# Optimization experiments

Hardware: AMD Instinct MI355X
Metric: run time of the kernel (lower is better)

## Reference

```python
import jax, jax.numpy as jnp
import numpy as np

S, HID = 2048, 4096
H, KV, D = 32, 8, 128
EPS = 1e-6
THETA = 10000.0


def setup_inputs() -> dict:
    key = jax.random.key(0)
    k0, k1, k2 = jax.random.split(key, 3)
    return {
        "positions": jnp.arange(S, dtype=jnp.int32),
        "hidden_states": jax.random.normal(k0, (S, HID), jnp.float32),
        "w_qkv": jax.random.normal(k1, ((H + 2 * KV) * D, HID), jnp.float32) * 0.02,
        "w_o": jax.random.normal(k2, (HID, H * D), jnp.float32) * 0.02,
        "gq": jnp.ones((D,), jnp.float32),
        "gk": jnp.ones((D,), jnp.float32),
    }


def _rmsnorm(x, g):
    # per-head RMSNorm over last dim (head_dim)
    return x * jax.lax.rsqrt(jnp.mean(x * x, axis=-1, keepdims=True) + EPS) * g


def _rope(x, positions):
    # NeoX-style rotary embedding, rotary_dim == head_dim
    half = D // 2
    inv_freq = 1.0 / (THETA ** (jnp.arange(half, dtype=jnp.float32) * 2.0 / D))
    freqs = positions.astype(jnp.float32)[:, None] * inv_freq  # [S, half]
    cos = jnp.cos(freqs)[:, None, :]  # [S, 1, half]
    sin = jnp.sin(freqs)[:, None, :]
    x1, x2 = x[..., :half], x[..., half:]
    return jnp.concatenate([x1 * cos - x2 * sin, x2 * cos + x1 * sin], axis=-1)


def reference(positions, hidden_states, w_qkv, w_o, gq, gk):
    qkv = hidden_states @ w_qkv.T  # [S, (H+2KV)*D]
    q = qkv[:, : H * D].reshape(S, H, D)
    k = qkv[:, H * D : (H + KV) * D].reshape(S, KV, D)
    v = qkv[:, (H + KV) * D :].reshape(S, KV, D)

    q = _rmsnorm(q, gq)
    k = _rmsnorm(k, gk)
    q = _rope(q, positions)
    k = _rope(k, positions)

    rep = H // KV
    kf = jnp.repeat(k, rep, axis=1)  # [S, H, D]
    vf = jnp.repeat(v, rep, axis=1)

    scale = D ** -0.5
    scores = jnp.einsum("qhd,khd->hqk", q, kf) * scale  # [H, S, S]
    causal = jnp.tril(jnp.ones((S, S), dtype=bool))
    scores = jnp.where(causal[None], scores, jnp.finfo(scores.dtype).min)
    attn = jax.nn.softmax(scores, axis=-1)
    ctx = jnp.einsum("hqk,khd->qhd", attn, vf).reshape(S, H * D)
    return ctx @ w_o.T  # [S, HID]
```

## Files before the change

### kernel.cpp

```cpp
#include <hip/hip_runtime.h>
#include <hip/hip_bf16.h>

#define S_LEN 2048
#define HID   4096
#define NH    32
#define NKV   8
#define DH    128
#define NQKV  ((NH + 2*NKV) * DH)

typedef __attribute__((ext_vector_type(8))) short s16x8;
typedef __attribute__((ext_vector_type(4))) short s16x4;
typedef __attribute__((ext_vector_type(4))) float f32x4;

__device__ __forceinline__ short f2bf(float x) {
    union { __hip_bfloat16 b; short s; } u;
    u.b = __float2bfloat16(x);
    return u.s;
}
__device__ __forceinline__ float bf2f(short s) {
    union { unsigned int u; float f; } v;
    v.u = ((unsigned int)(unsigned short)s) << 16;
    return v.f;
}

__device__ __forceinline__ void gload16(const void* g, void* l) {
    __builtin_amdgcn_global_load_lds(
        (const __attribute__((address_space(1))) void*)g,
        (__attribute__((address_space(3))) void*)l,
        16, 0, 0);
}

__device__ __forceinline__ void cstore(float* p, float v) { *p = v; }
__device__ __forceinline__ void cstore(short* p, float v) { *p = f2bf(v); }

#define ROPE_C (13.287712379549449f / 64.0f)

__global__ __launch_bounds__(256) void convert_hs_wqkv(
        const float* __restrict__ hs, short* __restrict__ hsp,
        const float* __restrict__ wq, short* __restrict__ wqb,
        const int* __restrict__ pos, float* __restrict__ cst)
{
    const int bid = blockIdx.x;
    if (bid < 1536) {
        const long n = (long)NQKV * HID;
        long i0 = ((long)bid * 256 + threadIdx.x) * 4;
        long stride = 1536L * 256 * 4;
        for (long i = i0; i < n; i += stride) {
            float4 v = *(const float4*)(wq + i);
            s16x4 o;
            o[0] = f2bf(v.x); o[1] = f2bf(v.y); o[2] = f2bf(v.z); o[3] = f2bf(v.w);
            *(s16x4*)(wqb + i) = o;
        }
        return;
    }
    if (bid < 2048) {
        const int nchunk = (S_LEN / 16) * (HID / 32) * 64;
        for (int c = (bid - 1536) * 256 + threadIdx.x; c < nchunk; c += 512 * 256) {
            int lane = c & 63, k32 = (c >> 6) & 127, m16 = c >> 13;
            int row = m16 * 16 + (lane & 15);
            int k   = k32 * 32 + (lane >> 4) * 8;
            const float4* p = (const float4*)(hs + (long)row * HID + k);
            float4 v0 = p[0], v1 = p[1];
            s16x8 o;
            o[0] = f2bf(v0.x); o[1] = f2bf(v0.y); o[2] = f2bf(v0.z); o[3] = f2bf(v0.w);
            o[4] = f2bf(v1.x); o[5] = f2bf(v1.y); o[6] = f2bf(v1.z); o[7] = f2bf(v1.w);
            *(s16x8*)(hsp + (long)c * 8) = o;
        }
        return;
    }
    const int idx = (bid - 2048) * 256 + threadIdx.x;
    const int s = idx >> 3, j0 = (idx & 7) * 8;
    const float po = (float)pos[s];
#pragma unroll
    for (int jj = 0; jj < 8; ++jj) {
        int j = j0 + jj;
        float ang = po * exp2f(-(float)j * ROPE_C);
        float2 cs;
        cs.x = cosf(ang);
        cs.y = sinf(ang);
        *(float2*)(cst + ((long)s * 64 + j) * 2) = cs;
    }
}

template <typename OT>
__global__ __launch_bounds__(256, 2) void gemm192(
        const short* __restrict__ Ap, const short* __restrict__ B,
        OT* __restrict__ C, int M, int N, int K)
{
    __shared__ char lds[49152];
    const int t = threadIdx.x;
    const int w = t >> 6, l = t & 63, g = l >> 4, q16 = l & 15;
    const int wm = w >> 1, wn = w & 1;
    const int bx = blockIdx.x, by = blockIdx.y;
    const int NT = K >> 6;

    const int srow = t >> 3;
    const int schunk = (t & 7) ^ (srow & 7);
    unsigned goffB[6];
#pragma unroll
    for (int i = 0; i < 6; ++i)
        goffB[i] = (unsigned)(((bx * 192 + i * 32 + srow) * K) * 2 + schunk * 16);
    const int dstw = w * 1024;

    auto STAGE = [&](int kt) {
        char* dB = lds + (kt & 1) * 24576 + dstw;
        const unsigned kb = (unsigned)kt * 128;
#pragma unroll
        for (int i = 0; i < 6; ++i)
            gload16((const char*)B + (goffB[i] + kb), dB + i * 4096);
    };

    unsigned aBase[4];
#pragma unroll
    for (int mi = 0; mi < 4; ++mi)
        aBase[mi] = ((unsigned)((by * 8 + wm * 4 + mi) * 128) * 64 + (unsigned)l) * 16;

    int boff[6];
#pragma unroll
    for (int ni = 0; ni < 6; ++ni) boff[ni] = (wn * 96 + ni * 16 + q16) * 128;
    const int sw0 = ((g) ^ (q16 & 7)) << 4;
    const int sw1 = ((4 + g) ^ (q16 & 7)) << 4;

    f32x4 acc[4][6] = {};
    s16x8 aE[4][2], aO[4][2], b0E[2][2], b0O[2][2], b1[4][2];

    STAGE(0);
    __builtin_amdgcn_sched_barrier(0);
#pragma unroll
    for (int mi = 0; mi < 4; ++mi)
#pragma unroll
        for (int kk = 0; kk < 2; ++kk)
            aE[mi][kk] = *(const s16x8*)((const char*)Ap + aBase[mi] + kk * 1024);
    __builtin_amdgcn_sched_barrier(0);
    STAGE(1);
    asm volatile("s_waitcnt vmcnt(6)" ::: "memory");
    __builtin_amdgcn_s_barrier();
    {
        const char* B0 = lds;
#pragma unroll
        for (int ni = 0; ni < 2; ++ni) {
            b0E[ni][0] = *(const s16x8*)(B0 + boff[ni] + sw0);
            b0E[ni][1] = *(const s16x8*)(B0 + boff[ni] + sw1);
        }
        asm volatile("s_waitcnt lgkmcnt(0)" ::: "memory");
        __builtin_amdgcn_sched_barrier(0);
    }

#define GB(KT, AC, AN, B0C, B0N, PAR) do {                                    \
                    \
    const char* Bc_ = lds + (PAR) * 24576;                                    \
    _Pragma("unroll")                                                         \
    for (int ni = 0; ni < 4; ++ni) {                                          \
        b1[ni][0] = *(const s16x8*)(Bc_ + boff[2 + ni] + sw0);                \
        b1[ni][1] = *(const s16x8*)(Bc_ + boff[2 + ni] + sw1);                \
    }                                                                         \
    __builtin_amdgcn_sched_barrier(0);                                        \
    __builtin_amdgcn_s_setprio(1);                                            \
    _Pragma("unroll")                                                         \
    for (int mi = 0; mi < 4; ++mi)                                            \
    _Pragma("unroll")                                                         \
    for (int ni = 0; ni < 2; ++ni)                                            \
    _Pragma("unroll")                                                         \
    for (int kk = 0; kk < 2; ++kk)                                            \
        acc[mi][ni] = __builtin_amdgcn_mfma_f32_16x16x32_bf16(                \
                AC[mi][kk], B0C[ni][kk], acc[mi][ni], 0, 0, 0);               \
    __builtin_amdgcn_s_setprio(0);                                            \
               \
    asm volatile("s_waitcnt lgkmcnt(0)" ::: "memory");                        \
    __builtin_amdgcn_sched_barrier(0);                                        \
    asm volatile("s_waitcnt vmcnt(0)" ::: "memory");                          \
    __builtin_amdgcn_s_barrier();                                             \
         \
    if ((KT) + 1 < NT) {                                                      \
        _Pragma("unroll")                                                     \
        for (int mi = 0; mi < 4; ++mi)                                        \
        _Pragma("unroll")                                                     \
        for (int kk = 0; kk < 2; ++kk)                                        \
            AN[mi][kk] = *(const s16x8*)((const char*)Ap + aBase[mi]          \
                    + (((KT) + 1) * 2 + kk) * 1024);                          \
    }                                                                         \
    __builtin_amdgcn_sched_barrier(0);                                        \
    if ((KT) + 2 < NT) STAGE((KT) + 2);                                       \
    if ((KT) + 1 < NT) {                                                      \
        const char* Bn_ = lds + ((PAR) ^ 1) * 24576;                          \
        _Pragma("unroll")                                                     \
        for (int ni = 0; ni < 2; ++ni) {                                      \
            B0N[ni][0] = *(const s16x8*)(Bn_ + boff[ni] + sw0);               \
            B0N[ni][1] = *(const s16x8*)(Bn_ + boff[ni] + sw1);               \
        }                                                                     \
    }                                                                         \
    __builtin_amdgcn_sched_barrier(0);                                        \
                                             \
    __builtin_amdgcn_s_setprio(1);                                            \
    _Pragma("unroll")                                                         \
    for (int mi = 0; mi < 4; ++mi)                                            \
    _Pragma("unroll")                                                         \
    for (int ni = 0; ni < 4; ++ni)                                            \
    _Pragma("unroll")                                                         \
    for (int kk = 0; kk < 2; ++kk)                                            \
        acc[mi][2 + ni] = __builtin_amdgcn_mfma_f32_16x16x32_bf16(            \
                AC[mi][kk], b1[ni][kk], acc[mi][2 + ni], 0, 0, 0);            \
    __builtin_amdgcn_s_setprio(0);                                            \
         \
    asm volatile("s_waitcnt lgkmcnt(0)" ::: "memory");                        \
    __builtin_amdgcn_sched_barrier(0);                                        \
    if ((KT) + 2 < NT) asm volatile("s_waitcnt vmcnt(6)" ::: "memory");       \
    else               asm volatile("s_waitcnt vmcnt(0)" ::: "memory");       \
    __builtin_amdgcn_sched_barrier(0);                                        \
} while (0)

    for (int kt = 0; kt < NT; kt += 2) {
        GB(kt,     aE, aO, b0E, b0O, 0);
        GB(kt + 1, aO, aE, b0O, b0E, 1);
    }
#undef GB

#pragma unroll
    for (int mi = 0; mi < 4; ++mi) {
        long row = (long)by * 128 + wm * 64 + mi * 16 + g * 4;
#pragma unroll
        for (int ni = 0; ni < 6; ++ni) {
            long col = (long)bx * 192 + wn * 96 + ni * 16 + q16;
            f32x4 v = acc[mi][ni];
#pragma unroll
            for (int r = 0; r < 4; ++r)
                cstore(&C[(row + r) * (long)N + col], v[r]);
        }
    }
}

template <typename OT>
__global__ __launch_bounds__(256, 2) void gemm_bt(
        const short* __restrict__ A, const short* __restrict__ B,
        OT* __restrict__ C, int M, int N, int K)
{
    __shared__ char lds[65536];
    const int t = threadIdx.x;
    const int w = t >> 6, l = t & 63, g = l >> 4, q16 = l & 15;
    const int wm = w >> 1, wn = w & 1;
    const int bx = blockIdx.x, by = blockIdx.y;
    const int NT = K >> 6;

    const int srow = t >> 3;
    const int schunk = (t & 7) ^ (srow & 7);
    unsigned goffA[4], goffB[4];
#pragma unroll
    for (int i = 0; i < 4; ++i) {
        goffA[i] = (unsigned)(((by * 128 + i * 32 + srow) * K) * 2 + schunk * 16);
        goffB[i] = (unsigned)(((bx * 128 + i * 32 + srow) * K) * 2 + schunk * 16);
    }
    const int dstw = w * 1024;

    auto STAGE = [&](int kt) {
        const int par = kt & 1;
        char* dA = lds + par * 16384 + dstw;
        char* dB = lds + 32768 + par * 16384 + dstw;
        const unsigned kb = (unsigned)kt * 128;
#pragma unroll
        for (int i = 0; i < 4; ++i) {
            gload16((const char*)A + (goffA[i] + kb), dA + i * 4096);
            gload16((const char*)B + (goffB[i] + kb), dB + i * 4096);
        }
    };

    int aoff[4], boff[4];
#pragma unroll
    for (int i = 0; i < 4; ++i) {
        aoff[i] = (wm * 64 + i * 16 + q16) * 128;
        boff[i] = (wn * 64 + i * 16 + q16) * 128;
    }
    const int sw0 = ((g) ^ (q16 & 7)) << 4;
    const int sw1 = ((4 + g) ^ (q16 & 7)) << 4;

    f32x4 acc[4][4] = {};
    s16x8 aE[4][2], aO[4][2], bf[4][2];

    STAGE(0); STAGE(1);
    asm volatile("s_waitcnt vmcnt(8)" ::: "memory");
    __builtin_amdgcn_s_barrier();
    {
        const char* A0 = lds;
#pragma unroll
        for (int mi = 0; mi < 4; ++mi) {
            aE[mi][0] = *(const s16x8*)(A0 + aoff[mi] + sw0);
            aE[mi][1] = *(const s16x8*)(A0 + aoff[mi] + sw1);
        }
    }

#define GB(KT, AC, AN, PAR) do {                                              \
    const char* Bs_ = lds + 32768 + (PAR) * 16384;                            \
    _Pragma("unroll")                                                         \
    for (int ni = 0; ni < 4; ++ni) {                                          \
        bf[ni][0] = *(const s16x8*)(Bs_ + boff[ni] + sw0);                    \
        bf[ni][1] = *(const s16x8*)(Bs_ + boff[ni] + sw1);                    \
    }                                                                         \
    asm volatile("s_waitcnt lgkmcnt(4)" ::: "memory");      \
    __builtin_amdgcn_sched_barrier(0);                                        \
    __builtin_amdgcn_s_setprio(1);                                            \
    _Pragma("unroll")                                                         \
    for (int mi = 0; mi < 4; ++mi)                                            \
    _Pragma("unroll")                                                         \
    for (int ni = 0; ni < 2; ++ni)                                            \
    _Pragma("unroll")                                                         \
    for (int kk = 0; kk < 2; ++kk)                                            \
        acc[mi][ni] = __builtin_amdgcn_mfma_f32_16x16x32_bf16(                \
                AC[mi][kk], bf[ni][kk], acc[mi][ni], 0, 0, 0);                \
    __builtin_amdgcn_s_setprio(0);                                            \
    asm volatile("s_waitcnt lgkmcnt(0)" ::: "memory");          \
    __builtin_amdgcn_sched_barrier(0);                                        \
    asm volatile("s_waitcnt vmcnt(0)" ::: "memory");        \
    __builtin_amdgcn_s_barrier();       \
    if ((KT) + 2 < NT) STAGE((KT) + 2);                                       \
    if ((KT) + 1 < NT) {                      \
        const char* An_ = lds + (((PAR) ^ 1) * 16384);                        \
        _Pragma("unroll")                                                     \
        for (int mi = 0; mi < 4; ++mi) {                                      \
            AN[mi][0] = *(const s16x8*)(An_ + aoff[mi] + sw0);                \
            AN[mi][1] = *(const s16x8*)(An_ + aoff[mi] + sw1);                \
        }                                                                     \
    }                                                                         \
    __builtin_amdgcn_s_setprio(1);                                            \
    _Pragma("unroll")                                                         \
    for (int mi = 0; mi < 4; ++mi)                                            \
    _Pragma("unroll")                                                         \
    for (int ni = 0; ni < 2; ++ni)                                            \
    _Pragma("unroll")                                                         \
    for (int kk = 0; kk < 2; ++kk)                                            \
        acc[mi][2 + ni] = __builtin_amdgcn_mfma_f32_16x16x32_bf16(            \
                AC[mi][kk], bf[2 + ni][kk], acc[mi][2 + ni], 0, 0, 0);        \
    __builtin_amdgcn_s_setprio(0);                                            \
} while (0)

    for (int kt = 0; kt < NT; kt += 2) {
        GB(kt,     aE, aO, 0);
        GB(kt + 1, aO, aE, 1);
    }
#undef GB

#pragma unroll
    for (int mi = 0; mi < 4; ++mi) {
        long row = (long)by * 128 + wm * 64 + mi * 16 + g * 4;
#pragma unroll
        for (int ni = 0; ni < 4; ++ni) {
            long col = (long)bx * 128 + wn * 64 + ni * 16 + q16;
            f32x4 v = acc[mi][ni];
#pragma unroll
            for (int r = 0; r < 4; ++r)
                cstore(&C[(row + r) * (long)N + col], v[r]);
        }
    }
}

__global__ __launch_bounds__(256) void post_gemm1_fused(
        const short* __restrict__ qkvb, const float* __restrict__ cst,
        const float* __restrict__ gk,
        short* __restrict__ ko, short* __restrict__ vt)
{
    const int bid = blockIdx.x;

    if (bid < 2048) {
        const int s = bid;
        const int slot = NH + (threadIdx.x >> 5);
        const int p = threadIdx.x & 31, d = p * 4;

        s16x4 xv = *(const s16x4*)(qkvb + (long)s * NQKV + slot * DH + d);
        float x[4];
#pragma unroll
        for (int r = 0; r < 4; ++r) x[r] = bf2f(xv[r]);

        float ss = x[0]*x[0] + x[1]*x[1] + x[2]*x[2] + x[3]*x[3];
#pragma unroll
        for (int o = 1; o < 32; o <<= 1) ss += __shfl_xor(ss, o);
        float rms = rsqrtf(ss * (1.0f / DH) + 1e-6f);

        float y[4];
#pragma unroll
        for (int r = 0; r < 4; ++r) y[r] = x[r] * rms * gk[d + r];

        float y2[4];
#pragma unroll
        for (int r = 0; r < 4; ++r) y2[r] = __shfl_xor(y[r], 16);

        const int jbase = d & 63;
        s16x4 ov;
#pragma unroll
        for (int r = 0; r < 4; ++r) {
            float2 cs = *(const float2*)(cst + ((long)s * 64 + jbase + r) * 2);
            float outv = (d < 64) ? (y[r] * cs.x - y2[r] * cs.y)
                                  : (y[r] * cs.x + y2[r] * cs.y);
            ov[r] = f2bf(outv);
        }
        *(s16x4*)(ko + ((long)s * NKV + (slot - NH)) * DH + d) = ov;
        return;
    }

    __shared__ short tile[64][72];
    const int idx2 = bid - 2048;
    const int sb = idx2 & 31, db = (idx2 >> 5) & 1, h = idx2 >> 6;
    const int t = threadIdx.x;
#pragma unroll
    for (int i = 0; i < 2; ++i) {
        int c = i * 256 + t;
        int row = c >> 3, dc = (c & 7) * 8;
        const short* src = qkvb + (long)(sb*64 + row) * NQKV
                           + (NH + NKV + h) * DH + db*64 + dc;
        s16x8 x = *(const s16x8*)src;
#pragma unroll
        for (int jj = 0; jj < 8; ++jj) tile[row][dc + jj] = x[jj];
    }
    __syncthreads();
#pragma unroll
    for (int i = 0; i < 2; ++i) {
        int c = i * 256 + t;
        int dr = c >> 3, sc = (c & 7) * 8;
        s16x8 y;
#pragma unroll
        for (int jj = 0; jj < 8; ++jj) y[jj] = tile[sc + jj][dr];
        short* dst = vt + (long)(h*DH + db*64 + dr) * S_LEN + sb*64 + sc;
        *(s16x8*)dst = y;
    }
}

__device__ __forceinline__ void stage_kv(const char* kgB, const char* vgB,
                                         int kt, int t, char* kd, char* vd)
{
    const int w = t >> 6;
#pragma unroll
    for (int ci = 0; ci < 4; ++ci) {
        int c = ci * 256 + t;
        int row = c >> 4, col16 = c & 15;
        const char* gk = kgB + (long)(kt*64 + row) * (NKV*DH*2)
                         + ((col16*16) ^ ((row & 7) << 4));
        gload16(gk, kd + ci*4096 + w*1024);
        int rowv = c >> 3, scol8 = c & 7;
        const char* gv = vgB + (long)rowv * (S_LEN*2) + kt*128
                         + ((scol8*16) ^ ((rowv & 7) << 4));
        gload16(gv, vd + ci*4096 + w*1024);
    }
}

__global__ __launch_bounds__(256, 2) void attn_kernel(
        const float* __restrict__ wo, short* __restrict__ wob,
        const short* __restrict__ qkvb, const float* __restrict__ cst,
        const float* __restrict__ gq,
        const short* __restrict__ kg, const short* __restrict__ vtg,
        short* __restrict__ ctx)
{
    const int bx = blockIdx.x;
    if (bx >= 512) {
        const long n = (long)HID * (NH * DH);
        long i0 = ((long)(bx - 512) * 256 + threadIdx.x) * 4;
        long stride = 2048L * 256 * 4;
        for (long i = i0; i < n; i += stride) {
            float4 v = *(const float4*)(wo + i);
            s16x4 o;
            o[0] = f2bf(v.x); o[1] = f2bf(v.y); o[2] = f2bf(v.z); o[3] = f2bf(v.w);
            *(s16x4*)(wob + i) = o;
        }
        return;
    }

    const int h  = bx & 31;
    const int slot = bx >> 5;
    const int qb = (slot < 8) ? slot : 23 - slot;
    const int kvh = h >> 2;
    const int t = threadIdx.x, w = t >> 6, l = t & 63, g = l >> 4, q16 = l & 15;

    __shared__ char Kl[2][16384];
    __shared__ char Vl[2][16384];
    __shared__ short Pl[4][32 * 64];

    const float scale = 0.08838834764831845f;
    const char* kgB = (const char*)kg + (long)kvh * DH * 2;
    const char* vgB = (const char*)vtg + (long)kvh * DH * (long)S_LEN * 2;

    const int nt = 2 * qb + 2;
    int qrow[2];
    qrow[0] = qb*128 + w*32 + q16;
    qrow[1] = qrow[0] + 16;

    stage_kv(kgB, vgB, 0, t, Kl[0], Vl[0]);

    s16x8 qf[2][4];
#pragma unroll
    for (int s = 0; s < 2; ++s) {
        const short* qptr = qkvb + (long)qrow[s] * NQKV + h * DH;
        s16x8 v0 = *(const s16x8*)(qptr + 0*32 + g*8);
        s16x8 v1 = *(const s16x8*)(qptr + 1*32 + g*8);
        s16x8 v2 = *(const s16x8*)(qptr + 2*32 + g*8);
        s16x8 v3 = *(const s16x8*)(qptr + 3*32 + g*8);
        float ssum = 0.f;
#pragma unroll
        for (int j = 0; j < 8; ++j) {
            float a = bf2f(v0[j]), b = bf2f(v1[j]);
            float c2 = bf2f(v2[j]), d2 = bf2f(v3[j]);
            ssum += a*a + b*b + c2*c2 + d2*d2;
        }
        ssum += __shfl_xor(ssum, 16);
        ssum += __shfl_xor(ssum, 32);
        float rms = rsqrtf(ssum * (1.0f / DH) + 1e-6f);
        const float* csp = cst + (long)qrow[s] * 128;
        s16x8 q0, q1, q2, q3;
#pragma unroll
        for (int j = 0; j < 8; ++j) {
            int jb0 = g*8 + j;
            float2 cs0 = *(const float2*)(csp + jb0 * 2);
            float y0 = bf2f(v0[j]) * rms * gq[jb0];
            float y2 = bf2f(v2[j]) * rms * gq[jb0 + 64];
            q0[j] = f2bf(y0 * cs0.x - y2 * cs0.y);
            q2[j] = f2bf(y2 * cs0.x + y0 * cs0.y);
            int jb1 = 32 + g*8 + j;
            float2 cs1 = *(const float2*)(csp + jb1 * 2);
            float y1 = bf2f(v1[j]) * rms * gq[jb1];
            float y3 = bf2f(v3[j]) * rms * gq[jb1 + 64];
            q1[j] = f2bf(y1 * cs1.x - y3 * cs1.y);
            q3[j] = f2bf(y3 * cs1.x + y1 * cs1.y);
        }
        qf[s][0] = q0; qf[s][1] = q1; qf[s][2] = q2; qf[s][3] = q3;
    }

    f32x4 oacc[2][8] = {};
    float m_run[2] = {-1e30f, -1e30f}, l_run[2] = {0.f, 0.f};

    __syncthreads();

    for (int kt = 0; kt < nt; ++kt) {
        const int b = kt & 1;
        if (kt + 1 < nt)
            stage_kv(kgB, vgB, kt + 1, t, Kl[b ^ 1], Vl[b ^ 1]);
        const char* kb = Kl[b];
        const char* vbb = Vl[b];

        f32x4 sacc[2][4] = {};
        __builtin_amdgcn_s_setprio(1);
#pragma unroll
        for (int m = 0; m < 4; ++m) {
            int kvr = m*16 + q16;
            s16x8 af[4];
#pragma unroll
            for (int dk = 0; dk < 4; ++dk) {
                int byte = (kvr*256 + (dk*32 + g*8)*2) ^ ((kvr & 7) << 4);
                af[dk] = *(const s16x8*)(kb + byte);
            }
#pragma unroll
            for (int s = 0; s < 2; ++s)
#pragma unroll
                for (int dk = 0; dk < 4; ++dk)
                    sacc[s][m] = __builtin_amdgcn_mfma_f32_16x16x32_bf16(
                            af[dk], qf[s][dk], sacc[s][m], 0,0,0);
        }
        __builtin_amdgcn_s_setprio(0);

        const bool diag = (kt >= 2*qb);
        float mx[2];
#pragma unroll
        for (int s = 0; s < 2; ++s) {
            mx[s] = -1e30f;
#pragma unroll
            for (int m = 0; m < 4; ++m)
#pragma unroll
                for (int r = 0; r < 4; ++r) {
                    float x = sacc[s][m][r] * scale;
                    if (diag) {
                        int kv = kt*64 + m*16 + g*4 + r;
                        if (kv > qrow[s]) x = -1e30f;
                    }
                    sacc[s][m][r] = x;
                    mx[s] = fmaxf(mx[s], x);
                }
            mx[s] = fmaxf(mx[s], __shfl_xor(mx[s], 16));
            mx[s] = fmaxf(mx[s], __shfl_xor(mx[s], 32));
        }
        if (__any((mx[0] > m_run[0] + 8.f) || (mx[1] > m_run[1] + 8.f))) {
#pragma unroll
            for (int s = 0; s < 2; ++s) {
                float m_new = fmaxf(m_run[s], mx[s]);
                float corr = __expf(m_run[s] - m_new);
                l_run[s] *= corr;
                m_run[s] = m_new;
                float rf[4];
#pragma unroll
                for (int r = 0; r < 4; ++r)
                    rf[r] = __shfl(corr, (g << 4) | (g*4 + r));
#pragma unroll
                for (int nf = 0; nf < 8; ++nf)
#pragma unroll
                    for (int r = 0; r < 4; ++r) oacc[s][nf][r] *= rf[r];
            }
        }
#pragma unroll
        for (int s = 0; s < 2; ++s) {
            float psum = 0.f;
#pragma unroll
            for (int m = 0; m < 4; ++m) {
                s16x4 pk;
#pragma unroll
                for (int r = 0; r < 4; ++r) {
                    float e = __expf(sacc[s][m][r] - m_run[s]);
                    psum += e;
                    pk[r] = f2bf(e);
                }
                int byte = ((s*16 + q16)*128 + (m*16 + g*4)*2) ^ ((q16 & 7) << 4);
                *(s16x4*)((char*)&Pl[w][0] + byte) = pk;
            }
            psum += __shfl_xor(psum, 16);
            psum += __shfl_xor(psum, 32);
            l_run[s] += psum;
        }

        __builtin_amdgcn_s_setprio(1);
#pragma unroll
        for (int ks = 0; ks < 2; ++ks) {
            s16x8 pa[2];
#pragma unroll
            for (int s = 0; s < 2; ++s) {
                int pbyte = ((s*16 + q16)*128 + (ks*32 + g*8)*2) ^ ((q16 & 7) << 4);
                pa[s] = *(const s16x8*)((const char*)&Pl[w][0] + pbyte);
            }
#pragma unroll
            for (int nf = 0; nf < 8; ++nf) {
                int drow = nf*16 + q16;
                int vbyte = (drow*128 + (ks*32 + g*8)*2) ^ ((drow & 7) << 4);
                s16x8 vbf = *(const s16x8*)(vbb + vbyte);
#pragma unroll
                for (int s = 0; s < 2; ++s)
                    oacc[s][nf] = __builtin_amdgcn_mfma_f32_16x16x32_bf16(
                            pa[s], vbf, oacc[s][nf], 0,0,0);
            }
        }
        __builtin_amdgcn_s_setprio(0);
        __syncthreads();
    }

    short* ot = (short*)&Kl[0][0];
#pragma unroll
    for (int s = 0; s < 2; ++s) {
        float lr[4];
#pragma unroll
        for (int r = 0; r < 4; ++r)
            lr[r] = __shfl(l_run[s], (g << 4) | (g*4 + r));
#pragma unroll
        for (int nf = 0; nf < 8; ++nf)
#pragma unroll
            for (int r = 0; r < 4; ++r) {
                int row = w*32 + s*16 + g*4 + r;
                int col = nf*16 + q16;
                ot[row * 128 + col] = f2bf(oacc[s][nf][r] / lr[r]);
            }
    }
    __syncthreads();
#pragma unroll
    for (int p = 0; p < 8; ++p) {
        int row = p * 16 + (t >> 4);
        int c8  = (t & 15) * 8;
        s16x8 v = *(const s16x8*)(ot + row * 128 + c8);
        *(s16x8*)(ctx + (long)(qb*128 + row) * (NH*DH) + h*DH + c8) = v;
    }
}

extern "C" void kernel_launch(void* const* d_in, const int* in_sizes, int n_in,
                              void* d_out, int out_size, void* d_ws, size_t ws_size,
                              hipStream_t stream)
{
    const int*   positions = (const int*)  d_in[0];
    const float* hs        = (const float*)d_in[1];
    const float* wqkv      = (const float*)d_in[2];
    const float* wo        = (const float*)d_in[3];
    const float* gq        = (const float*)d_in[4];
    const float* gk        = (const float*)d_in[5];
    float* out = (float*)d_out;
    char* ws = (char*)d_ws;

    const size_t MB = 1ull << 20;
    short* hsb   = (short*)(ws);
    short* ctxb  = (short*)(ws);
    short* wqkvb = (short*)(ws + 16*MB);
    short* wob   = (short*)(ws + 16*MB);
    short* vtbuf = (short*)(ws + 48*MB);
    short* qkvb  = (short*)(ws + 67*MB);
    float* cst   = (float*)(ws + 91*MB);
    short* kbuf  = (short*)(ws + 107*MB);

    (void)in_sizes; (void)n_in; (void)out_size; (void)ws_size;

    convert_hs_wqkv<<<2112, 256, 0, stream>>>(hs, hsb, wqkv, wqkvb,
                                              positions, cst);
    gemm192<short><<<dim3(NQKV/192, S_LEN/128), 256, 0, stream>>>(
            hsb, wqkvb, qkvb, S_LEN, NQKV, HID);
    post_gemm1_fused<<<2560, 256, 0, stream>>>(
            qkvb, cst, gk, kbuf, vtbuf);
    attn_kernel<<<dim3(2560), 256, 0, stream>>>(
            wo, wob, qkvb, cst, gq, kbuf, vtbuf, ctxb);
    gemm_bt<float><<<dim3(HID/128, S_LEN/128), 256, 0, stream>>>(
            ctxb, wob, out, S_LEN, HID, HID);
}
```

Before: 286.3 us.

## Store ctx in MFMA-fragment-packed layout and load GEMM A operand directly from global

The attention kernel now writes its context output in a pre-packed layout that matches the per-lane MFMA A-fragment order. The output-projection GEMM then loads its A operand straight from global memory into registers instead of staging it through LDS. This halves LDS use, which may allow higher occupancy, and removes A-side LDS traffic. B fragments are split into two halves that are software-pipelined with new waitcnt placement. The cost is that A-operand global latency is exposed per iteration, and the packed layout must exactly match the fragment mapping the GEMM expects.

```diff
diff --git a/kernel.cpp b/kernel.cpp
--- a/kernel.cpp
+++ b/kernel.cpp
@@ -231,10 +231,10 @@
 
 template <typename OT>
 __global__ __launch_bounds__(256, 2) void gemm_bt(
-        const short* __restrict__ A, const short* __restrict__ B,
+        const short* __restrict__ Ap, const short* __restrict__ B,
         OT* __restrict__ C, int M, int N, int K)
 {
-    __shared__ char lds[65536];
+    __shared__ char lds[32768];
     const int t = threadIdx.x;
     const int w = t >> 6, l = t & 63, g = l >> 4, q16 = l & 15;
     const int wm = w >> 1, wn = w & 1;
@@ -243,58 +243,64 @@
 
     const int srow = t >> 3;
     const int schunk = (t & 7) ^ (srow & 7);
-    unsigned goffA[4], goffB[4];
-#pragma unroll
-    for (int i = 0; i < 4; ++i) {
-        goffA[i] = (unsigned)(((by * 128 + i * 32 + srow) * K) * 2 + schunk * 16);
+    unsigned goffB[4];
+#pragma unroll
+    for (int i = 0; i < 4; ++i)
         goffB[i] = (unsigned)(((bx * 128 + i * 32 + srow) * K) * 2 + schunk * 16);
-    }
     const int dstw = w * 1024;
 
     auto STAGE = [&](int kt) {
-        const int par = kt & 1;
-        char* dA = lds + par * 16384 + dstw;
-        char* dB = lds + 32768 + par * 16384 + dstw;
+        char* dB = lds + (kt & 1) * 16384 + dstw;
         const unsigned kb = (unsigned)kt * 128;
 #pragma unroll
-        for (int i = 0; i < 4; ++i) {
-            gload16((const char*)A + (goffA[i] + kb), dA + i * 4096);
+        for (int i = 0; i < 4; ++i)
             gload16((const char*)B + (goffB[i] + kb), dB + i * 4096);
-        }
     };
 
-    int aoff[4], boff[4];
-#pragma unroll
-    for (int i = 0; i < 4; ++i) {
-        aoff[i] = (wm * 64 + i * 16 + q16) * 128;
-        boff[i] = (wn * 64 + i * 16 + q16) * 128;
-    }
+    unsigned aBase[4];
+#pragma unroll
+    for (int mi = 0; mi < 4; ++mi)
+        aBase[mi] = ((unsigned)((by * 8 + wm * 4 + mi) * 128) * 64 + (unsigned)l) * 16;
+
+    int boff[4];
+#pragma unroll
+    for (int ni = 0; ni < 4; ++ni) boff[ni] = (wn * 64 + ni * 16 + q16) * 128;
     const int sw0 = ((g) ^ (q16 & 7)) << 4;
     const int sw1 = ((4 + g) ^ (q16 & 7)) << 4;
 
     f32x4 acc[4][4] = {};
-    s16x8 aE[4][2], aO[4][2], bf[4][2];
-
-    STAGE(0); STAGE(1);
-    asm volatile("s_waitcnt vmcnt(8)" ::: "memory");
+    s16x8 aE[4][2], aO[4][2], b0E[2][2], b0O[2][2], b1[2][2];
+
+    STAGE(0);
+    __builtin_amdgcn_sched_barrier(0);
+#pragma unroll
+    for (int mi = 0; mi < 4; ++mi)
+#pragma unroll
+        for (int kk = 0; kk < 2; ++kk)
+            aE[mi][kk] = *(const s16x8*)((const char*)Ap + aBase[mi] + kk * 1024);
+    __builtin_amdgcn_sched_barrier(0);
+    STAGE(1);
+    asm volatile("s_waitcnt vmcnt(4)" ::: "memory");
     __builtin_amdgcn_s_barrier();
     {
-        const char* A0 = lds;
-#pragma unroll
-        for (int mi = 0; mi < 4; ++mi) {
-            aE[mi][0] = *(const s16x8*)(A0 + aoff[mi] + sw0);
-            aE[mi][1] = *(const s16x8*)(A0 + aoff[mi] + sw1);
-        }
-    }
-
-#define GB(KT, AC, AN, PAR) do {                                              \
-    const char* Bs_ = lds + 32768 + (PAR) * 16384;                            \
-    _Pragma("unroll")                                                         \
-    for (int ni = 0; ni < 4; ++ni) {                                          \
-        bf[ni][0] = *(const s16x8*)(Bs_ + boff[ni] + sw0);                    \
-        bf[ni][1] = *(const s16x8*)(Bs_ + boff[ni] + sw1);                    \
+        const char* B0 = lds;
+#pragma unroll
+        for (int ni = 0; ni < 2; ++ni) {
+            b0E[ni][0] = *(const s16x8*)(B0 + boff[ni] + sw0);
+            b0E[ni][1] = *(const s16x8*)(B0 + boff[ni] + sw1);
+        }
+        asm volatile("s_waitcnt lgkmcnt(0)" ::: "memory");
+        __builtin_amdgcn_sched_barrier(0);
+    }
+
+#define GB2(KT, AC, AN, B0C, B0N, PAR) do {                                   \
+                    \
+    const char* Bc_ = lds + (PAR) * 16384;                                    \
+    _Pragma("unroll")                                                         \
+    for (int ni = 0; ni < 2; ++ni) {                                          \
+        b1[ni][0] = *(const s16x8*)(Bc_ + boff[2 + ni] + sw0);                \
+        b1[ni][1] = *(const s16x8*)(Bc_ + boff[2 + ni] + sw1);                \
     }                                                                         \
-    asm volatile("s_waitcnt lgkmcnt(4)" ::: "memory");      \
     __builtin_amdgcn_sched_barrier(0);                                        \
     __builtin_amdgcn_s_setprio(1);                                            \
     _Pragma("unroll")                                                         \
@@ -304,21 +310,34 @@
     _Pragma("unroll")                                                         \
     for (int kk = 0; kk < 2; ++kk)                                            \
         acc[mi][ni] = __builtin_amdgcn_mfma_f32_16x16x32_bf16(                \
-                AC[mi][kk], bf[ni][kk], acc[mi][ni], 0, 0, 0);                \
+                AC[mi][kk], B0C[ni][kk], acc[mi][ni], 0, 0, 0);               \
     __builtin_amdgcn_s_setprio(0);                                            \
-    asm volatile("s_waitcnt lgkmcnt(0)" ::: "memory");          \
-    __builtin_amdgcn_sched_barrier(0);                                        \
-    asm volatile("s_waitcnt vmcnt(0)" ::: "memory");        \
-    __builtin_amdgcn_s_barrier();       \
+               \
+    asm volatile("s_waitcnt lgkmcnt(0)" ::: "memory");                        \
+    __builtin_amdgcn_sched_barrier(0);                                        \
+    asm volatile("s_waitcnt vmcnt(0)" ::: "memory");                          \
+    __builtin_amdgcn_s_barrier();                                             \
+         \
+    if ((KT) + 1 < NT) {                                                      \
+        _Pragma("unroll")                                                     \
+        for (int mi = 0; mi < 4; ++mi)                                        \
+        _Pragma("unroll")                                                     \
+        for (int kk = 0; kk < 2; ++kk)                                        \
+            AN[mi][kk] = *(const s16x8*)((const char*)Ap + aBase[mi]          \
+                    + (((KT) + 1) * 2 + kk) * 1024);                          \
+    }                                                                         \
+    __builtin_amdgcn_sched_barrier(0);                                        \
     if ((KT) + 2 < NT) STAGE((KT) + 2);                                       \
-    if ((KT) + 1 < NT) {                      \
-        const char* An_ = lds + (((PAR) ^ 1) * 16384);                        \
+    if ((KT) + 1 < NT) {                                                      \
+        const char* Bn_ = lds + ((PAR) ^ 1) * 16384;                          \
         _Pragma("unroll")                                                     \
-        for (int mi = 0; mi < 4; ++mi) {                                      \
-            AN[mi][0] = *(const s16x8*)(An_ + aoff[mi] + sw0);                \
-            AN[mi][1] = *(const s16x8*)(An_ + aoff[mi] + sw1);                \
+        for (int ni = 0; ni < 2; ++ni) {                                      \
+            B0N[ni][0] = *(const s16x8*)(Bn_ + boff[ni] + sw0);               \
+            B0N[ni][1] = *(const s16x8*)(Bn_ + boff[ni] + sw1);               \
         }                                                                     \
     }                                                                         \
+    __builtin_amdgcn_sched_barrier(0);                                        \
+                                             \
     __builtin_amdgcn_s_setprio(1);                                            \
     _Pragma("unroll")                                                         \
     for (int mi = 0; mi < 4; ++mi)                                            \
@@ -327,15 +346,21 @@
     _Pragma("unroll")                                                         \
     for (int kk = 0; kk < 2; ++kk)                                            \
         acc[mi][2 + ni] = __builtin_amdgcn_mfma_f32_16x16x32_bf16(            \
-                AC[mi][kk], bf[2 + ni][kk], acc[mi][2 + ni], 0, 0, 0);        \
+                AC[mi][kk], b1[ni][kk], acc[mi][2 + ni], 0, 0, 0);            \
     __builtin_amdgcn_s_setprio(0);                                            \
+         \
+    asm volatile("s_waitcnt lgkmcnt(0)" ::: "memory");                        \
+    __builtin_amdgcn_sched_barrier(0);                                        \
+    if ((KT) + 2 < NT) asm volatile("s_waitcnt vmcnt(4)" ::: "memory");       \
+    else               asm volatile("s_waitcnt vmcnt(0)" ::: "memory");       \
+    __builtin_amdgcn_sched_barrier(0);                                        \
 } while (0)
 
     for (int kt = 0; kt < NT; kt += 2) {
-        GB(kt,     aE, aO, 0);
-        GB(kt + 1, aO, aE, 1);
-    }
-#undef GB
+        GB2(kt,     aE, aO, b0E, b0O, 0);
+        GB2(kt + 1, aO, aE, b0O, b0E, 1);
+    }
+#undef GB2
 
 #pragma unroll
     for (int mi = 0; mi < 4; ++mi) {
@@ -444,7 +469,7 @@
         const short* __restrict__ qkvb, const float* __restrict__ cst,
         const float* __restrict__ gq,
         const short* __restrict__ kg, const short* __restrict__ vtg,
-        short* __restrict__ ctx)
+        short* __restrict__ ctxp)
 {
     const int bx = blockIdx.x;
     if (bx >= 512) {
@@ -651,10 +676,13 @@
     __syncthreads();
 #pragma unroll
     for (int p = 0; p < 8; ++p) {
-        int row = p * 16 + (t >> 4);
-        int c8  = (t & 15) * 8;
-        s16x8 v = *(const s16x8*)(ot + row * 128 + c8);
-        *(s16x8*)(ctx + (long)(qb*128 + row) * (NH*DH) + h*DH + c8) = v;
+        int cc = p * 256 + t;
+        int m16l = cc >> 8, k32l = (cc >> 6) & 3, lane = cc & 63;
+        int row = m16l * 16 + (lane & 15);
+        int col8 = k32l * 32 + (lane >> 4) * 8;
+        s16x8 v = *(const s16x8*)(ot + row * 128 + col8);
+        long gc = ((long)(qb * 8 + m16l) * 128 + (h * 4 + k32l)) * 64 + lane;
+        *(s16x8*)(ctxp + gc * 8) = v;
     }
 }
 
```

After: 289.4 us. Within noise of the previous version (+1.1%).
